# Optimization experiments

Measured on AMD Instinct MI355X. Metric: run time of the kernel, lower is better.

Reference implementation:

```python
import jax, jax.numpy as jnp
import numpy as np

N = 262144   # collocation points
D = 64       # hidden_dim
E_S = 2      # shared experts per layer
E_R = 4      # routed experts per layer (6 total - 2 shared)
K = 2        # top_k
L = 3        # MoE layers


def _init(key, shape, fan_in):
    return jax.random.normal(key, shape, jnp.float32) / np.float32(np.sqrt(fan_in))


def setup_inputs() -> dict:
    key = jax.random.key(0)
    ks = jax.random.split(key, 16)
    return {
        "x": jax.random.normal(ks[0], (N, 1), jnp.float32),
        "t": jax.random.normal(ks[1], (N, 1), jnp.float32),
        "W_in": _init(ks[2], (2, D), 2),
        "b_in": jnp.zeros((D,), jnp.float32),
        # stacked over [layer, expert, ...]
        "sW1": _init(ks[3], (L, E_S, D, D), D),
        "sb1": jnp.zeros((L, E_S, D), jnp.float32),
        "sW2": _init(ks[4], (L, E_S, D, D), D),
        "sb2": jnp.zeros((L, E_S, D), jnp.float32),
        "rW1": _init(ks[5], (L, E_R, D, D), D),
        "rb1": jnp.zeros((L, E_R, D), jnp.float32),
        "rW2": _init(ks[6], (L, E_R, D, D), D),
        "rb2": jnp.zeros((L, E_R, D), jnp.float32),
        "routW": _init(ks[7], (L, D, E_R), D),
        "routb": jnp.zeros((L, E_R), jnp.float32),
        "W_out": _init(ks[8], (D, 1), D),
        "b_out": jnp.zeros((1,), jnp.float32),
    }


def _moe_layer(h, sW1, sb1, sW2, sb2, rW1, rb1, rW2, rb2, routW, routb):
    # shared experts: all run on every token, summed
    sh = jnp.tanh(jnp.einsum('nd,edh->neh', h, sW1) + sb1)       # [N,E_S,D]
    shared_out = jnp.einsum('neh,eho->no', sh, sW2) + sb2.sum(0)  # [N,D]
    # router: full softmax weights, top-k scatter mask (NOT renormalized)
    logits = h @ routW + routb                                    # [N,E_R]
    rw = jax.nn.softmax(logits, axis=1)
    _, top_idx = jax.lax.top_k(rw, K)                             # [N,K]
    mask = jax.nn.one_hot(top_idx, E_R, dtype=rw.dtype).sum(axis=1)  # [N,E_R]
    weight = rw * mask                                            # [N,E_R]
    # routed experts computed densely over all tokens, weighted-summed
    rh = jnp.tanh(jnp.einsum('nd,edh->neh', h, rW1) + rb1)        # [N,E_R,D]
    r_out = jnp.einsum('neh,eho->neo', rh, rW2) + rb2             # [N,E_R,D]
    routed_out = jnp.einsum('ne,neo->no', weight, r_out)          # [N,D]
    return shared_out + routed_out


def reference(x, t, W_in, b_in, sW1, sb1, sW2, sb2, rW1, rb1, rW2, rb2, routW, routb, W_out, b_out):
    xt = jnp.concatenate([x, t], axis=1)                          # [N,2]
    h = jnp.tanh(xt @ W_in + b_in)                                # [N,D]
    for l in range(L):
        h_moe = _moe_layer(h, sW1[l], sb1[l], sW2[l], sb2[l],
                           rW1[l], rb1[l], rW2[l], rb2[l], routW[l], routb[l])
        h = jnp.tanh(h + h_moe)
    return h @ W_out + b_out                                      # [N,1]
```

## Files before the change

### kernel.cpp

```cpp
#include <hip/hip_runtime.h>


typedef __attribute__((ext_vector_type(8))) short bf16x8;
typedef __attribute__((ext_vector_type(4))) float f32x4;

#define MFMA16(A, B, C) __builtin_amdgcn_mfma_f32_16x16x32_bf16((A), (B), (C), 0, 0, 0)

namespace {
constexpr int D = 64, ES = 2, ER = 4, NL = 3;
constexpr int BLK = 256;
constexpr int T = 2;
constexpr int TOKPB = 4 * T * 16;
constexpr unsigned HM = 0xFFFF0000u;

__device__ __forceinline__ float tanh_fast(float x) {
  x = fminf(15.f, fmaxf(-15.f, x));
  const float e = __expf(2.f * x);
  return 1.f - 2.f * __builtin_amdgcn_rcpf(e + 1.f);
}

__device__ __forceinline__ void split3(float v, short& a, short& b, short& c) {
  const unsigned u0 = __builtin_bit_cast(unsigned, v);
  a = (short)(u0 >> 16);
  const float r1 = v - __builtin_bit_cast(float, u0 & HM);
  const unsigned u1 = __builtin_bit_cast(unsigned, r1);
  b = (short)(u1 >> 16);
  const float r2 = r1 - __builtin_bit_cast(float, u1 & HM);
  c = (short)(__builtin_bit_cast(unsigned, r2) >> 16);
}

__device__ __forceinline__ void build_b3(const f32x4 s0, const f32x4 s1,
                                         bf16x8& b0, bf16x8& b1, bf16x8& b2) {
  #pragma unroll
  for (int j = 0; j < 4; ++j) { short a,b,c; split3(s0[j],a,b,c); b0[j]=a;   b1[j]=b;   b2[j]=c; }
  #pragma unroll
  for (int j = 0; j < 4; ++j) { short a,b,c; split3(s1[j],a,b,c); b0[4+j]=a; b1[4+j]=b; b2[4+j]=c; }
}

__device__ __forceinline__ void stage_w(const float* __restrict__ W, bf16x8* wf, int tid) {
  #pragma unroll
  for (int rep = 0; rep < 2; ++rep) {
    const int slot = tid + rep * BLK;
    const int f = slot >> 6, ln = slot & 63;
    const int mt = f >> 1, ks = f & 1;
    const int m  = (ln & 15) + (mt << 4);
    const int kb = (ks << 5) + ((ln >> 4) << 2);
    float v[8];
    #pragma unroll
    for (int e = 0; e < 8; ++e) {
      const int k = kb + ((e >> 2) << 4) + (e & 3);
      v[e] = W[k * D + m];
    }
    bf16x8 h0, h1, h2;
    #pragma unroll
    for (int e = 0; e < 8; ++e) { short a,b,c; split3(v[e],a,b,c); h0[e]=a; h1[e]=b; h2[e]=c; }
    wf[(f*3 + 0)*64 + ln] = h0;
    wf[(f*3 + 1)*64 + ln] = h1;
    wf[(f*3 + 2)*64 + ln] = h2;
  }
}

__device__ __forceinline__ void run_mfma6(const bf16x8* wf, int lane,
                                          const bf16x8 (&B)[3][T][2], f32x4 (&acc)[T][4]) {
  #pragma unroll
  for (int mt = 0; mt < 4; ++mt) {
    bf16x8 A0[2], A1[2], A2[2];
    #pragma unroll
    for (int ks = 0; ks < 2; ++ks) {
      const int f = mt*2 + ks;
      A0[ks] = wf[(f*3 + 0)*64 + lane];
      A1[ks] = wf[(f*3 + 1)*64 + lane];
      A2[ks] = wf[(f*3 + 2)*64 + lane];
    }
    #pragma unroll
    for (int tt = 0; tt < T; ++tt)
      #pragma unroll
      for (int ks = 0; ks < 2; ++ks) {
        f32x4 c = acc[tt][mt];
        c = MFMA16(A0[ks], B[0][tt][ks], c);
        c = MFMA16(A0[ks], B[1][tt][ks], c);
        c = MFMA16(A1[ks], B[0][tt][ks], c);
        c = MFMA16(A0[ks], B[2][tt][ks], c);
        c = MFMA16(A1[ks], B[1][tt][ks], c);
        c = MFMA16(A2[ks], B[0][tt][ks], c);
        acc[tt][mt] = c;
      }
  }
}

__device__ __forceinline__ void expert_pass(
    const float* __restrict__ W1, const float* __restrict__ b1,
    const float* __restrict__ W2, const float* __restrict__ b2,
    const bf16x8 (&hB)[3][T][2], const float (&wet)[T],
    f32x4 (&moe)[T][4], bf16x8* wf, int tid, int lane, int g) {
  __syncthreads();
  stage_w(W1, wf, tid);
  __syncthreads();
  f32x4 a1[T][4];
  #pragma unroll
  for (int mt = 0; mt < 4; ++mt) {
    const f32x4 bb = *(const f32x4*)(b1 + (mt << 4) + (g << 2));
    #pragma unroll
    for (int tt = 0; tt < T; ++tt) a1[tt][mt] = bb;
  }
  run_mfma6(wf, lane, hB, a1);
  bf16x8 uB[3][T][2];
  #pragma unroll
  for (int tt = 0; tt < T; ++tt) {
    #pragma unroll
    for (int mt = 0; mt < 4; ++mt)
      #pragma unroll
      for (int r = 0; r < 4; ++r) a1[tt][mt][r] = wet[tt] * tanh_fast(a1[tt][mt][r]);
    #pragma unroll
    for (int ks = 0; ks < 2; ++ks)
      build_b3(a1[tt][2*ks], a1[tt][2*ks+1], uB[0][tt][ks], uB[1][tt][ks], uB[2][tt][ks]);
  }
  __syncthreads();
  stage_w(W2, wf, tid);
  __syncthreads();
  #pragma unroll
  for (int mt = 0; mt < 4; ++mt) {
    const f32x4 bb = *(const f32x4*)(b2 + (mt << 4) + (g << 2));
    #pragma unroll
    for (int tt = 0; tt < T; ++tt)
      #pragma unroll
      for (int r = 0; r < 4; ++r) moe[tt][mt][r] += wet[tt] * bb[r];
  }
  run_mfma6(wf, lane, uB, moe);
}
}

__global__ __launch_bounds__(BLK, 2)
void pinn_moe_mfma(const float* __restrict__ x, const float* __restrict__ t,
                   const float* __restrict__ Win, const float* __restrict__ bin,
                   const float* __restrict__ sW1, const float* __restrict__ sb1,
                   const float* __restrict__ sW2, const float* __restrict__ sb2,
                   const float* __restrict__ rW1, const float* __restrict__ rb1,
                   const float* __restrict__ rW2, const float* __restrict__ rb2,
                   const float* __restrict__ routW, const float* __restrict__ routb,
                   const float* __restrict__ Wout, const float* __restrict__ bout,
                   float* __restrict__ out) {
  __shared__ bf16x8 wf[8 * 3 * 64];
  const int tid = threadIdx.x;
  const int wid = tid >> 6, lane = tid & 63;
  const int l15 = lane & 15, g = lane >> 4;
  int tb[T];
  #pragma unroll
  for (int tt = 0; tt < T; ++tt) tb[tt] = blockIdx.x * TOKPB + wid * (T * 16) + tt * 16;

  f32x4 hacc[T][4];

  #pragma unroll
  for (int tt = 0; tt < T; ++tt) {
    const float xv = x[tb[tt] + l15], tv = t[tb[tt] + l15];
    #pragma unroll
    for (int mt = 0; mt < 4; ++mt) {
      const f32x4 w0 = *(const f32x4*)(Win + (mt << 4) + (g << 2));
      const f32x4 w1 = *(const f32x4*)(Win + D + (mt << 4) + (g << 2));
      const f32x4 bb = *(const f32x4*)(bin + (mt << 4) + (g << 2));
      #pragma unroll
      for (int r = 0; r < 4; ++r)
        hacc[tt][mt][r] = tanh_fast(fmaf(xv, w0[r], fmaf(tv, w1[r], bb[r])));
    }
  }

  for (int l = 0; l < NL; ++l) {
    bf16x8 hB[3][T][2];
    #pragma unroll
    for (int tt = 0; tt < T; ++tt)
      #pragma unroll
      for (int ks = 0; ks < 2; ++ks)
        build_b3(hacc[tt][2*ks], hacc[tt][2*ks+1], hB[0][tt][ks], hB[1][tt][ks], hB[2][tt][ks]);

    f32x4 moe[T][4];
    #pragma unroll
    for (int tt = 0; tt < T; ++tt)
      #pragma unroll
      for (int mt = 0; mt < 4; ++mt)
        #pragma unroll
        for (int r = 0; r < 4; ++r) moe[tt][mt][r] = 0.f;

    const float one[T] = {1.f, 1.f};
    for (int e = 0; e < ES; ++e) {
      const size_t o = (size_t)(l * ES + e);
      expert_pass(sW1 + o*D*D, sb1 + o*D, sW2 + o*D*D, sb2 + o*D,
                  hB, one, moe, wf, tid, lane, g);
    }

    f32x4 wsel[T];
    {
      const float* rWp = routW + (size_t)l * D * ER;
      const f32x4 rb = *(const f32x4*)(routb + l * ER);
      #pragma unroll
      for (int tt = 0; tt < T; ++tt) {
        f32x4 lg = rb;
        #pragma unroll
        for (int mt = 0; mt < 4; ++mt)
          #pragma unroll
          for (int r = 0; r < 4; ++r) {
            const f32x4 w4 = *(const f32x4*)(rWp + ((mt << 4) + (g << 2) + r) * ER);
            const float hv = hacc[tt][mt][r];
            #pragma unroll
            for (int e = 0; e < 4; ++e) lg[e] = fmaf(hv, w4[e], lg[e]);
          }
        #pragma unroll
        for (int e = 0; e < 4; ++e) {
          float vv = lg[e];
          vv += __shfl_xor(vv, 16);
          vv += __shfl_xor(vv, 32);
          lg[e] = vv;
        }
        const float mx = fmaxf(fmaxf(lg[0], lg[1]), fmaxf(lg[2], lg[3]));
        f32x4 p; float s = 0.f;
        #pragma unroll
        for (int e = 0; e < 4; ++e) { p[e] = __expf(lg[e] - mx); s += p[e]; }
        const float inv = 1.f / s;
        #pragma unroll
        for (int e = 0; e < 4; ++e) p[e] *= inv;
        #pragma unroll
        for (int a = 0; a < 4; ++a) {
          int rank = 0;
          #pragma unroll
          for (int f2 = 0; f2 < 4; ++f2)
            if (f2 != a) rank += ((p[f2] > p[a]) || (p[f2] == p[a] && f2 < a)) ? 1 : 0;
          wsel[tt][a] = (rank < 2) ? p[a] : 0.f;
        }
      }
    }

    for (int e = 0; e < ER; ++e) {
      float wet[T];
      #pragma unroll
      for (int tt = 0; tt < T; ++tt) {
        float w = wsel[tt][0];
        w = (e == 1) ? wsel[tt][1] : w;
        w = (e == 2) ? wsel[tt][2] : w;
        w = (e == 3) ? wsel[tt][3] : w;
        wet[tt] = w;
      }
      const size_t o = (size_t)(l * ER + e);
      expert_pass(rW1 + o*D*D, rb1 + o*D, rW2 + o*D*D, rb2 + o*D,
                  hB, wet, moe, wf, tid, lane, g);
    }

    #pragma unroll
    for (int tt = 0; tt < T; ++tt)
      #pragma unroll
      for (int mt = 0; mt < 4; ++mt)
        #pragma unroll
        for (int r = 0; r < 4; ++r)
          hacc[tt][mt][r] = tanh_fast(hacc[tt][mt][r] + moe[tt][mt][r]);
  }

  const float bo = bout[0];
  #pragma unroll
  for (int tt = 0; tt < T; ++tt) {
    float o = 0.f;
    #pragma unroll
    for (int mt = 0; mt < 4; ++mt) {
      const f32x4 w = *(const f32x4*)(Wout + (mt << 4) + (g << 2));
      #pragma unroll
      for (int r = 0; r < 4; ++r) o = fmaf(hacc[tt][mt][r], w[r], o);
    }
    o += __shfl_xor(o, 16);
    o += __shfl_xor(o, 32);
    o += bo;
    if (g == 0) out[tb[tt] + l15] = o;
  }
}

extern "C" void kernel_launch(void* const* d_in, const int* in_sizes, int n_in,
                              void* d_out, int out_size, void* d_ws, size_t ws_size,
                              hipStream_t stream) {
  (void)n_in; (void)d_ws; (void)ws_size; (void)out_size;
  const float* x     = (const float*)d_in[0];
  const float* t     = (const float*)d_in[1];
  const float* Win   = (const float*)d_in[2];
  const float* bin   = (const float*)d_in[3];
  const float* sW1   = (const float*)d_in[4];
  const float* sb1   = (const float*)d_in[5];
  const float* sW2   = (const float*)d_in[6];
  const float* sb2   = (const float*)d_in[7];
  const float* rW1   = (const float*)d_in[8];
  const float* rb1   = (const float*)d_in[9];
  const float* rW2   = (const float*)d_in[10];
  const float* rb2   = (const float*)d_in[11];
  const float* routW = (const float*)d_in[12];
  const float* routb = (const float*)d_in[13];
  const float* Wout  = (const float*)d_in[14];
  const float* bout  = (const float*)d_in[15];
  float* out = (float*)d_out;

  const int n = in_sizes[0];
  const int grid = n / TOKPB;
  pinn_moe_mfma<<<dim3(grid), dim3(BLK), 0, stream>>>(
      x, t, Win, bin, sW1, sb1, sW2, sb2, rW1, rb1, rW2, rb2,
      routW, routb, Wout, bout, out);
}
```

Baseline: 517.2 us.

## Pre-split weights once and double-buffer async global-to-LDS weight fragment loads

Adds a prologue kernel that converts every expert weight matrix into the 3-way bf16-split MFMA fragment layout in workspace, so the main kernel no longer redoes the split per block. The main kernel streams these fragments into a double-buffered LDS area with global_load_lds, prefetching the next matrix while MFMAs run on the current one. It also caches biases and router weights in LDS and raises wave priority around MFMA sections. The cost is an extra launch and more LDS per block, which could reduce occupancy.

Result: faster. 475.0 us (-8.1%).

```diff
diff --git a/kernel.cpp b/kernel.cpp
--- a/kernel.cpp
+++ b/kernel.cpp
@@ -1,4 +1,5 @@
 #include <hip/hip_runtime.h>
+#include <cstdint>
 
 
 typedef __attribute__((ext_vector_type(8))) short bf16x8;
@@ -11,6 +12,13 @@
 constexpr int BLK = 256;
 constexpr int T = 2;
 constexpr int TOKPB = 4 * T * 16;
+constexpr int NMAT = NL * 6 * 2;
+constexpr int MATB = 8 * 3 * 64;
+constexpr int MATBYTES = MATB * 16;
+constexpr int CST_BIAS = 0;
+constexpr int CST_RW   = NMAT * 64;
+constexpr int CST_RB   = CST_RW + NL * D * ER;
+constexpr int CST_N    = CST_RB + 16;
 constexpr unsigned HM = 0xFFFF0000u;
 
 __device__ __forceinline__ float tanh_fast(float x) {
@@ -37,31 +45,9 @@
   for (int j = 0; j < 4; ++j) { short a,b,c; split3(s1[j],a,b,c); b0[4+j]=a; b1[4+j]=b; b2[4+j]=c; }
 }
 
-__device__ __forceinline__ void stage_w(const float* __restrict__ W, bf16x8* wf, int tid) {
-  #pragma unroll
-  for (int rep = 0; rep < 2; ++rep) {
-    const int slot = tid + rep * BLK;
-    const int f = slot >> 6, ln = slot & 63;
-    const int mt = f >> 1, ks = f & 1;
-    const int m  = (ln & 15) + (mt << 4);
-    const int kb = (ks << 5) + ((ln >> 4) << 2);
-    float v[8];
-    #pragma unroll
-    for (int e = 0; e < 8; ++e) {
-      const int k = kb + ((e >> 2) << 4) + (e & 3);
-      v[e] = W[k * D + m];
-    }
-    bf16x8 h0, h1, h2;
-    #pragma unroll
-    for (int e = 0; e < 8; ++e) { short a,b,c; split3(v[e],a,b,c); h0[e]=a; h1[e]=b; h2[e]=c; }
-    wf[(f*3 + 0)*64 + ln] = h0;
-    wf[(f*3 + 1)*64 + ln] = h1;
-    wf[(f*3 + 2)*64 + ln] = h2;
-  }
-}
-
-__device__ __forceinline__ void run_mfma6(const bf16x8* wf, int lane,
+__device__ __forceinline__ void run_mfma6(const bf16x8* __restrict__ wf, int lane,
                                           const bf16x8 (&B)[3][T][2], f32x4 (&acc)[T][4]) {
+  __builtin_amdgcn_s_setprio(1);
   #pragma unroll
   for (int mt = 0; mt < 4; ++mt) {
     bf16x8 A0[2], A1[2], A2[2];
@@ -86,70 +72,86 @@
         acc[tt][mt] = c;
       }
   }
-}
-
-__device__ __forceinline__ void expert_pass(
-    const float* __restrict__ W1, const float* __restrict__ b1,
-    const float* __restrict__ W2, const float* __restrict__ b2,
-    const bf16x8 (&hB)[3][T][2], const float (&wet)[T],
-    f32x4 (&moe)[T][4], bf16x8* wf, int tid, int lane, int g) {
-  __syncthreads();
-  stage_w(W1, wf, tid);
-  __syncthreads();
-  f32x4 a1[T][4];
-  #pragma unroll
-  for (int mt = 0; mt < 4; ++mt) {
-    const f32x4 bb = *(const f32x4*)(b1 + (mt << 4) + (g << 2));
-    #pragma unroll
-    for (int tt = 0; tt < T; ++tt) a1[tt][mt] = bb;
-  }
-  run_mfma6(wf, lane, hB, a1);
-  bf16x8 uB[3][T][2];
-  #pragma unroll
-  for (int tt = 0; tt < T; ++tt) {
-    #pragma unroll
-    for (int mt = 0; mt < 4; ++mt)
-      #pragma unroll
-      for (int r = 0; r < 4; ++r) a1[tt][mt][r] = wet[tt] * tanh_fast(a1[tt][mt][r]);
-    #pragma unroll
-    for (int ks = 0; ks < 2; ++ks)
-      build_b3(a1[tt][2*ks], a1[tt][2*ks+1], uB[0][tt][ks], uB[1][tt][ks], uB[2][tt][ks]);
-  }
-  __syncthreads();
-  stage_w(W2, wf, tid);
-  __syncthreads();
-  #pragma unroll
-  for (int mt = 0; mt < 4; ++mt) {
-    const f32x4 bb = *(const f32x4*)(b2 + (mt << 4) + (g << 2));
-    #pragma unroll
-    for (int tt = 0; tt < T; ++tt)
-      #pragma unroll
-      for (int r = 0; r < 4; ++r) moe[tt][mt][r] += wet[tt] * bb[r];
-  }
-  run_mfma6(wf, lane, uB, moe);
-}
-}
+  __builtin_amdgcn_s_setprio(0);
+}
+
+typedef const __attribute__((address_space(1))) unsigned int* as1u;
+typedef __attribute__((address_space(3))) unsigned int* as3u;
+__device__ __forceinline__ void gld_lds16(const void* g, const void* l) {
+  __builtin_amdgcn_global_load_lds((as1u)(uintptr_t)g,
+                                   (as3u)(unsigned int)(uintptr_t)l, 16, 0, 0);
+}
+}
+
+__global__ __launch_bounds__(256) void split_weights_k(
+    const float* __restrict__ sW1, const float* __restrict__ sW2,
+    const float* __restrict__ rW1, const float* __restrict__ rW2,
+    bf16x8* __restrict__ wsf) {
+  const int mat = blockIdx.x;
+  const int l = mat / 12, r = mat % 12, e = r >> 1, wch = r & 1;
+  const float* W = (e < ES) ? ((wch ? sW2 : sW1) + (size_t)(l*ES + e) * D * D)
+                            : ((wch ? rW2 : rW1) + (size_t)(l*ER + (e-ES)) * D * D);
+  const int tid = threadIdx.x;
+  bf16x8* dst = wsf + (size_t)mat * MATB;
+  #pragma unroll
+  for (int rep = 0; rep < 2; ++rep) {
+    const int slot = tid + rep * 256;
+    const int f = slot >> 6, ln = slot & 63;
+    const int mt = f >> 1, ks = f & 1;
+    const int m  = (ln & 15) + (mt << 4);
+    const int kb = (ks << 5) + ((ln >> 4) << 2);
+    bf16x8 h0, h1, h2;
+    #pragma unroll
+    for (int e8 = 0; e8 < 8; ++e8) {
+      const int k = kb + ((e8 >> 2) << 4) + (e8 & 3);
+      short a, b, c; split3(W[k * D + m], a, b, c);
+      h0[e8] = a; h1[e8] = b; h2[e8] = c;
+    }
+    dst[(f*3 + 0)*64 + ln] = h0;
+    dst[(f*3 + 1)*64 + ln] = h1;
+    dst[(f*3 + 2)*64 + ln] = h2;
+  }
+}
+
+#define SYNC_LGKM_BAR() do { asm volatile("s_waitcnt lgkmcnt(0)" ::: "memory"); \
+                             __builtin_amdgcn_s_barrier(); } while (0)
+#define WAIT6_BAR()     do { asm volatile("s_waitcnt vmcnt(6)" ::: "memory");   \
+                             __builtin_amdgcn_s_barrier(); } while (0)
 
 __global__ __launch_bounds__(BLK, 2)
-void pinn_moe_mfma(const float* __restrict__ x, const float* __restrict__ t,
-                   const float* __restrict__ Win, const float* __restrict__ bin,
-                   const float* __restrict__ sW1, const float* __restrict__ sb1,
-                   const float* __restrict__ sW2, const float* __restrict__ sb2,
-                   const float* __restrict__ rW1, const float* __restrict__ rb1,
-                   const float* __restrict__ rW2, const float* __restrict__ rb2,
-                   const float* __restrict__ routW, const float* __restrict__ routb,
-                   const float* __restrict__ Wout, const float* __restrict__ bout,
-                   float* __restrict__ out) {
-  __shared__ bf16x8 wf[8 * 3 * 64];
-  const int tid = threadIdx.x;
-  const int wid = tid >> 6, lane = tid & 63;
+void pinn_moe_mfma2(const float* __restrict__ x, const float* __restrict__ t,
+                    const float* __restrict__ Win, const float* __restrict__ bin,
+                    const float* __restrict__ sb1, const float* __restrict__ sb2,
+                    const float* __restrict__ rb1, const float* __restrict__ rb2,
+                    const float* __restrict__ routW, const float* __restrict__ routb,
+                    const float* __restrict__ Wout, const float* __restrict__ bout,
+                    const bf16x8* __restrict__ wsf, float* __restrict__ out) {
+  __shared__ bf16x8 wfrag[2][MATB];
+  __shared__ float  cst[CST_N];
+  const int tid = threadIdx.x, wid = tid >> 6, lane = tid & 63;
   const int l15 = lane & 15, g = lane >> 4;
+
+  {
+    const char* gb = (const char*)wsf + (size_t)0 * MATBYTES + wid * 1024 + lane * 16;
+    const char* lb = (const char*)&wfrag[0][0] + wid * 1024;
+    #pragma unroll
+    for (int rep = 0; rep < 6; ++rep) gld_lds16(gb + rep * 4096, lb + rep * 4096);
+  }
+
+  for (int i = tid; i < NMAT * 64; i += BLK) {
+    const int mI = i >> 6, j = i & 63;
+    const int ll = mI / 12, rr = mI % 12, ee = rr >> 1, ww = rr & 1;
+    const float* bp = (ee < ES) ? ((ww ? sb2 : sb1) + (ll*ES + ee) * D)
+                                : ((ww ? rb2 : rb1) + (ll*ER + (ee-ES)) * D);
+    cst[CST_BIAS + i] = bp[j];
+  }
+  for (int i = tid; i < NL * D * ER; i += BLK) cst[CST_RW + i] = routW[i];
+  if (tid < NL * ER) cst[CST_RB + tid] = routb[tid];
+
   int tb[T];
   #pragma unroll
-  for (int tt = 0; tt < T; ++tt) tb[tt] = blockIdx.x * TOKPB + wid * (T * 16) + tt * 16;
-
+  for (int tt = 0; tt < T; ++tt) tb[tt] = blockIdx.x * TOKPB + wid * (T*16) + tt * 16;
   f32x4 hacc[T][4];
-
   #pragma unroll
   for (int tt = 0; tt < T; ++tt) {
     const float xv = x[tb[tt] + l15], tv = t[tb[tt] + l15];
@@ -164,6 +166,9 @@
     }
   }
 
+  SYNC_LGKM_BAR();
+
+  #pragma unroll 1
   for (int l = 0; l < NL; ++l) {
     bf16x8 hB[3][T][2];
     #pragma unroll
@@ -172,6 +177,43 @@
       for (int ks = 0; ks < 2; ++ks)
         build_b3(hacc[tt][2*ks], hacc[tt][2*ks+1], hB[0][tt][ks], hB[1][tt][ks], hB[2][tt][ks]);
 
+    f32x4 wsel[T];
+    #pragma unroll
+    for (int tt = 0; tt < T; ++tt) {
+      f32x4 lg = *(const f32x4*)&cst[CST_RB + l * ER];
+      #pragma unroll
+      for (int mt = 0; mt < 4; ++mt)
+        #pragma unroll
+        for (int r = 0; r < 4; ++r) {
+          const f32x4 w4 = *(const f32x4*)&cst[CST_RW + l*D*ER + ((mt<<4)+(g<<2)+r)*ER];
+          const float hv = hacc[tt][mt][r];
+          #pragma unroll
+          for (int e = 0; e < 4; ++e) lg[e] = fmaf(hv, w4[e], lg[e]);
+        }
+      #pragma unroll
+      for (int e = 0; e < 4; ++e) {
+        float vv = lg[e];
+        vv += __shfl_xor(vv, 16);
+        vv += __shfl_xor(vv, 32);
+        lg[e] = vv;
+      }
+      const float mx = fmaxf(fmaxf(lg[0], lg[1]), fmaxf(lg[2], lg[3]));
+      f32x4 p; float s = 0.f;
+      #pragma unroll
+      for (int e = 0; e < 4; ++e) { p[e] = __expf(lg[e] - mx); s += p[e]; }
+      const float inv = 1.f / s;
+      #pragma unroll
+      for (int e = 0; e < 4; ++e) p[e] *= inv;
+      #pragma unroll
+      for (int a = 0; a < 4; ++a) {
+        int rank = 0;
+        #pragma unroll
+        for (int f2 = 0; f2 < 4; ++f2)
+          if (f2 != a) rank += ((p[f2] > p[a]) || (p[f2] == p[a] && f2 < a)) ? 1 : 0;
+        wsel[tt][a] = (rank < 2) ? p[a] : 0.f;
+      }
+    }
+
     f32x4 moe[T][4];
     #pragma unroll
     for (int tt = 0; tt < T; ++tt)
@@ -180,67 +222,72 @@
         #pragma unroll
         for (int r = 0; r < 4; ++r) moe[tt][mt][r] = 0.f;
 
-    const float one[T] = {1.f, 1.f};
-    for (int e = 0; e < ES; ++e) {
-      const size_t o = (size_t)(l * ES + e);
-      expert_pass(sW1 + o*D*D, sb1 + o*D, sW2 + o*D*D, sb2 + o*D,
-                  hB, one, moe, wf, tid, lane, g);
-    }
-
-    f32x4 wsel[T];
-    {
-      const float* rWp = routW + (size_t)l * D * ER;
-      const f32x4 rb = *(const f32x4*)(routb + l * ER);
+    #pragma unroll 1
+    for (int e = 0; e < 6; ++e) {
+      const int mm = (l*6 + e) * 2;
+      float wet[T];
       #pragma unroll
       for (int tt = 0; tt < T; ++tt) {
-        f32x4 lg = rb;
+        float w = 1.f;
+        if (e >= ES) {
+          w = wsel[tt][0];
+          w = (e == 3) ? wsel[tt][1] : w;
+          w = (e == 4) ? wsel[tt][2] : w;
+          w = (e == 5) ? wsel[tt][3] : w;
+        }
+        wet[tt] = w;
+      }
+
+      SYNC_LGKM_BAR();
+      {
+        const int nx = mm + 1;
+        const char* gb = (const char*)wsf + (size_t)nx * MATBYTES + wid * 1024 + lane * 16;
+        const char* lb = (const char*)&wfrag[1][0] + wid * 1024;
+        #pragma unroll
+        for (int rep = 0; rep < 6; ++rep) gld_lds16(gb + rep * 4096, lb + rep * 4096);
+      }
+      WAIT6_BAR();
+
+      f32x4 a1[T][4];
+      #pragma unroll
+      for (int mt = 0; mt < 4; ++mt) {
+        const f32x4 bb = *(const f32x4*)&cst[CST_BIAS + mm*64 + (mt << 4) + (g << 2)];
+        #pragma unroll
+        for (int tt = 0; tt < T; ++tt) a1[tt][mt] = bb;
+      }
+      run_mfma6(&wfrag[0][0], lane, hB, a1);
+
+      bf16x8 uB[3][T][2];
+      #pragma unroll
+      for (int tt = 0; tt < T; ++tt) {
         #pragma unroll
         for (int mt = 0; mt < 4; ++mt)
           #pragma unroll
-          for (int r = 0; r < 4; ++r) {
-            const f32x4 w4 = *(const f32x4*)(rWp + ((mt << 4) + (g << 2) + r) * ER);
-            const float hv = hacc[tt][mt][r];
-            #pragma unroll
-            for (int e = 0; e < 4; ++e) lg[e] = fmaf(hv, w4[e], lg[e]);
-          }
-        #pragma unroll
-        for (int e = 0; e < 4; ++e) {
-          float vv = lg[e];
-          vv += __shfl_xor(vv, 16);
-          vv += __shfl_xor(vv, 32);
-          lg[e] = vv;
-        }
-        const float mx = fmaxf(fmaxf(lg[0], lg[1]), fmaxf(lg[2], lg[3]));
-        f32x4 p; float s = 0.f;
-        #pragma unroll
-        for (int e = 0; e < 4; ++e) { p[e] = __expf(lg[e] - mx); s += p[e]; }
-        const float inv = 1.f / s;
-        #pragma unroll
-        for (int e = 0; e < 4; ++e) p[e] *= inv;
-        #pragma unroll
-        for (int a = 0; a < 4; ++a) {
-          int rank = 0;
+          for (int r = 0; r < 4; ++r) a1[tt][mt][r] = wet[tt] * tanh_fast(a1[tt][mt][r]);
+        #pragma unroll
+        for (int ks = 0; ks < 2; ++ks)
+          build_b3(a1[tt][2*ks], a1[tt][2*ks+1], uB[0][tt][ks], uB[1][tt][ks], uB[2][tt][ks]);
+      }
+
+      SYNC_LGKM_BAR();
+      {
+        const int nx = (mm + 2 < NMAT) ? mm + 2 : 0;
+        const char* gb = (const char*)wsf + (size_t)nx * MATBYTES + wid * 1024 + lane * 16;
+        const char* lb = (const char*)&wfrag[0][0] + wid * 1024;
+        #pragma unroll
+        for (int rep = 0; rep < 6; ++rep) gld_lds16(gb + rep * 4096, lb + rep * 4096);
+      }
+      WAIT6_BAR();
+
+      #pragma unroll
+      for (int mt = 0; mt < 4; ++mt) {
+        const f32x4 bb = *(const f32x4*)&cst[CST_BIAS + (mm+1)*64 + (mt << 4) + (g << 2)];
+        #pragma unroll
+        for (int tt = 0; tt < T; ++tt)
           #pragma unroll
-          for (int f2 = 0; f2 < 4; ++f2)
-            if (f2 != a) rank += ((p[f2] > p[a]) || (p[f2] == p[a] && f2 < a)) ? 1 : 0;
-          wsel[tt][a] = (rank < 2) ? p[a] : 0.f;
-        }
-      }
-    }
-
-    for (int e = 0; e < ER; ++e) {
-      float wet[T];
-      #pragma unroll
-      for (int tt = 0; tt < T; ++tt) {
-        float w = wsel[tt][0];
-        w = (e == 1) ? wsel[tt][1] : w;
-        w = (e == 2) ? wsel[tt][2] : w;
-        w = (e == 3) ? wsel[tt][3] : w;
-        wet[tt] = w;
-      }
-      const size_t o = (size_t)(l * ER + e);
-      expert_pass(rW1 + o*D*D, rb1 + o*D, rW2 + o*D*D, rb2 + o*D,
-                  hB, wet, moe, wf, tid, lane, g);
+          for (int r = 0; r < 4; ++r) moe[tt][mt][r] += wet[tt] * bb[r];
+      }
+      run_mfma6(&wfrag[1][0], lane, uB, moe);
     }
 
     #pragma unroll
@@ -267,12 +314,14 @@
     o += bo;
     if (g == 0) out[tb[tt] + l15] = o;
   }
+
+  asm volatile("s_waitcnt vmcnt(0)" ::: "memory");
 }
 
 extern "C" void kernel_launch(void* const* d_in, const int* in_sizes, int n_in,
                               void* d_out, int out_size, void* d_ws, size_t ws_size,
                               hipStream_t stream) {
-  (void)n_in; (void)d_ws; (void)ws_size; (void)out_size;
+  (void)n_in; (void)ws_size; (void)out_size;
   const float* x     = (const float*)d_in[0];
   const float* t     = (const float*)d_in[1];
   const float* Win   = (const float*)d_in[2];
@@ -291,9 +340,11 @@
   const float* bout  = (const float*)d_in[15];
   float* out = (float*)d_out;
 
+  bf16x8* wsf = (bf16x8*)d_ws;
+
+  split_weights_k<<<dim3(NMAT), dim3(256), 0, stream>>>(sW1, sW2, rW1, rW2, wsf);
+
   const int n = in_sizes[0];
-  const int grid = n / TOKPB;
-  pinn_moe_mfma<<<dim3(grid), dim3(BLK), 0, stream>>>(
-      x, t, Win, bin, sW1, sb1, sW2, sb2, rW1, rb1, rW2, rb2,
-      routW, routb, Wout, bout, out);
-}
+  pinn_moe_mfma2<<<dim3(n / TOKPB), dim3(BLK), 0, stream>>>(
+      x, t, Win, bin, sb1, sb2, rb1, rb2, routW, routb, Wout, bout, wsf, out);
+}
```
